# Kernel optimization log

Measured on AMD Instinct MI355X. Metric: run time of the kernel, lower is better.

## Reference

```python
import jax, jax.numpy as jnp
import numpy as np

B = 512          # batch of visual features
VF_D = 4096      # visual feature dim (VGG fc7)
HID_D = 2048     # hidden dim
EMB_D = 300      # order-embedding / label-vector dim
N_LABELS = 2000  # number of GT label vectors


def setup_inputs() -> dict:
    key = jax.random.key(0)
    ks = jax.random.split(key, 4)
    vfs = jax.random.normal(ks[0], (B, VF_D), dtype=jnp.float32)
    W1 = jax.random.normal(ks[1], (VF_D, HID_D), dtype=jnp.float32) * (1.0 / np.sqrt(VF_D))
    b1 = jnp.zeros((HID_D,), dtype=jnp.float32)
    W2 = jax.random.normal(ks[2], (HID_D, EMB_D), dtype=jnp.float32) * (1.0 / np.sqrt(HID_D))
    b2 = jnp.zeros((EMB_D,), dtype=jnp.float32)
    gt_label_vecs = jax.random.normal(ks[3], (N_LABELS, EMB_D), dtype=jnp.float32)
    return {"vfs": vfs, "W1": W1, "b1": b1, "W2": W2, "b2": b2,
            "gt_label_vecs": gt_label_vecs}


def reference(vfs, W1, b1, W2, b2, gt_label_vecs):
    # hidden_layer: ReLU -> (Dropout, identity at eval) -> Linear
    vf_hidden = jnp.dot(jax.nn.relu(vfs), W1) + b1            # [B, HID_D]
    # embedding_layer: ReLU -> Linear
    vf_emb = jnp.dot(jax.nn.relu(vf_hidden), W2) + b2         # [B, EMB_D]
    # order_sim(hypers=gt_label_vecs, hypos=vf_emb):
    #   score = -|| clamp(hypo - hyper, min=0) ||^2, batched over all pairs
    diff = jax.nn.relu(vf_emb[:, None, :] - gt_label_vecs[None, :, :])  # [B, N, D]
    score_stack = -jnp.sum(diff * diff, axis=-1)              # [B, N_LABELS]
    return score_stack, vf_emb
```

## Files before the change

### kernel.cpp

```cpp
#include <hip/hip_runtime.h>

#define B_SZ   512
#define VFD    4096
#define HIDD   2048
#define EMBD   300
#define NLAB   2000
#define NPAD   320

#define G1_SPLIT 4
#define G2_SPLIT 8

typedef __attribute__((ext_vector_type(8))) short short8x;
typedef __attribute__((ext_vector_type(4))) float f32x4;
typedef __attribute__((ext_vector_type(8))) unsigned short ushort8;
typedef __attribute__((ext_vector_type(4))) unsigned short ushort4x;

typedef const __attribute__((address_space(1))) unsigned int* gas_t;
typedef __attribute__((address_space(3))) unsigned int* las_t;

__device__ inline unsigned short f2bf(float x) {
    unsigned u = __float_as_uint(x);
    u += 0x7FFF + ((u >> 16) & 1);
    return (unsigned short)(u >> 16);
}

__global__ __launch_bounds__(256) void prep_kernel(
    const float* __restrict__ vfs, unsigned short* __restrict__ Xb,
    const float* __restrict__ W1, unsigned short* __restrict__ W1T,
    const float* __restrict__ W2, unsigned short* __restrict__ W2T)
{
    __shared__ float tile[64][65];
    const int tid = threadIdx.x;
    const int blk = blockIdx.x;

    if (blk < 1024) {
        const int i = (blk * 256 + tid) * 8;
        float4 a = *(const float4*)&vfs[i];
        float4 b = *(const float4*)&vfs[i + 4];
        ushort8 o;
        o[0] = f2bf(fmaxf(a.x, 0.f)); o[1] = f2bf(fmaxf(a.y, 0.f));
        o[2] = f2bf(fmaxf(a.z, 0.f)); o[3] = f2bf(fmaxf(a.w, 0.f));
        o[4] = f2bf(fmaxf(b.x, 0.f)); o[5] = f2bf(fmaxf(b.y, 0.f));
        o[6] = f2bf(fmaxf(b.z, 0.f)); o[7] = f2bf(fmaxf(b.w, 0.f));
        *(ushort8*)&Xb[i] = o;
        return;
    }

    const float* in; unsigned short* out; int N, ldK, bx, by;
    if (blk < 3072) {
        const int b = blk - 1024;
        in = W1; out = W1T; N = HIDD; ldK = VFD; bx = b & 31; by = b >> 5;
    } else {
        const int b = blk - 3072;
        in = W2; out = W2T; N = EMBD; ldK = HIDD; bx = b % 5; by = b / 5;
    }
    const int n0 = bx * 64, k0 = by * 64;

    #pragma unroll
    for (int i = 0; i < 4; ++i) {
        const int s = tid + 256 * i;
        const int kr = s >> 4, nc = (s & 15) * 4;
        float4 v = {0.f, 0.f, 0.f, 0.f};
        if (n0 + nc < N) v = *(const float4*)&in[(size_t)(k0 + kr) * N + n0 + nc];
        tile[kr][nc + 0] = v.x; tile[kr][nc + 1] = v.y;
        tile[kr][nc + 2] = v.z; tile[kr][nc + 3] = v.w;
    }
    __syncthreads();

    const int row = tid >> 2, kq = (tid & 3) * 16;
    ushort8 o0, o1;
    #pragma unroll
    for (int j = 0; j < 8; ++j) o0[j] = f2bf(tile[kq + j][row]);
    #pragma unroll
    for (int j = 0; j < 8; ++j) o1[j] = f2bf(tile[kq + 8 + j][row]);
    const size_t off = (size_t)(n0 + row) * ldK + k0 + kq;
    *(ushort8*)&out[off]     = o0;
    *(ushort8*)&out[off + 8] = o1;
}

template<int LDA, int LDB, int LDC, int KCHUNK>
__global__ __launch_bounds__(256) void gemm_bf16_kernel(
    const unsigned short* __restrict__ A,
    const unsigned short* __restrict__ Bt,
    float* __restrict__ Cpart, int M)
{
    __shared__ unsigned short As[2][2048];
    __shared__ unsigned short Bs[2][2048];

    const int tid = threadIdx.x;
    const int m0 = blockIdx.y * 64, n0 = blockIdx.x * 64;
    const int kbase = blockIdx.z * KCHUNK;

    const int soct = tid >> 6, srow = tid & 63;
    const unsigned short* ga = A  + (size_t)(m0 + srow) * LDA + kbase + soct * 8;
    const unsigned short* gb = Bt + (size_t)(n0 + srow) * LDB + kbase + soct * 8;

    const int lane = tid & 63;
    const int wave = tid >> 6;
    const int wm = (wave & 1) * 32;
    const int wn = (wave >> 1) * 32;
    const int q = lane >> 4, l15 = lane & 15;

    f32x4 acc00 = {0.f,0.f,0.f,0.f}, acc01 = {0.f,0.f,0.f,0.f};
    f32x4 acc10 = {0.f,0.f,0.f,0.f}, acc11 = {0.f,0.f,0.f,0.f};

    __builtin_amdgcn_global_load_lds((gas_t)(const void*)ga,
                                     (las_t)(void*)&As[0][tid * 8], 16, 0, 0);
    __builtin_amdgcn_global_load_lds((gas_t)(const void*)gb,
                                     (las_t)(void*)&Bs[0][tid * 8], 16, 0, 0);

    const int iters = KCHUNK / 32;
    for (int t = 0; t < iters; ++t) {
        const int cur = t & 1, nxt = cur ^ 1;
        __syncthreads();

        if (t + 1 < iters) {
            __builtin_amdgcn_global_load_lds((gas_t)(const void*)(ga + (t + 1) * 32),
                                             (las_t)(void*)&As[nxt][tid * 8], 16, 0, 0);
            __builtin_amdgcn_global_load_lds((gas_t)(const void*)(gb + (t + 1) * 32),
                                             (las_t)(void*)&Bs[nxt][tid * 8], 16, 0, 0);
        }

        short8x a0 = *(short8x*)&As[cur][(q * 64 + wm +      l15) * 8];
        short8x a1 = *(short8x*)&As[cur][(q * 64 + wm + 16 + l15) * 8];
        short8x b0 = *(short8x*)&Bs[cur][(q * 64 + wn +      l15) * 8];
        short8x b1 = *(short8x*)&Bs[cur][(q * 64 + wn + 16 + l15) * 8];
        acc00 = __builtin_amdgcn_mfma_f32_16x16x32_bf16(a0, b0, acc00, 0, 0, 0);
        acc01 = __builtin_amdgcn_mfma_f32_16x16x32_bf16(a0, b1, acc01, 0, 0, 0);
        acc10 = __builtin_amdgcn_mfma_f32_16x16x32_bf16(a1, b0, acc10, 0, 0, 0);
        acc11 = __builtin_amdgcn_mfma_f32_16x16x32_bf16(a1, b1, acc11, 0, 0, 0);
    }

    float* Cz = Cpart + (size_t)blockIdx.z * M * LDC;
    #pragma unroll
    for (int r = 0; r < 4; ++r) {
        const int rr = m0 + wm + q * 4 + r;
        const int cc = n0 + wn + l15;
        Cz[(size_t)rr * LDC + cc]             = acc00[r];
        Cz[(size_t)rr * LDC + cc + 16]        = acc01[r];
        Cz[(size_t)(rr + 16) * LDC + cc]      = acc10[r];
        Cz[(size_t)(rr + 16) * LDC + cc + 16] = acc11[r];
    }
}

__global__ __launch_bounds__(256) void reduce_h_kernel(
    const float* __restrict__ Hpart, const float* __restrict__ b1,
    unsigned short* __restrict__ Hb)
{
    const int i = (blockIdx.x * 256 + threadIdx.x) * 4;
    const int col = i & (HIDD - 1);
    float4 s = *(const float4*)&b1[col];
    #pragma unroll
    for (int z = 0; z < G1_SPLIT; ++z) {
        float4 p = *(const float4*)&Hpart[(size_t)z * B_SZ * HIDD + i];
        s.x += p.x; s.y += p.y; s.z += p.z; s.w += p.w;
    }
    ushort4x o;
    o[0] = f2bf(fmaxf(s.x, 0.f));
    o[1] = f2bf(fmaxf(s.y, 0.f));
    o[2] = f2bf(fmaxf(s.z, 0.f));
    o[3] = f2bf(fmaxf(s.w, 0.f));
    *(ushort4x*)&Hb[i] = o;
}

__global__ __launch_bounds__(256) void reduce_e_kernel(
    const float* __restrict__ Epart, const float* __restrict__ b2,
    float* __restrict__ E)
{
    const int gid = blockIdx.x * 256 + threadIdx.x;
    if (gid >= B_SZ * EMBD) return;
    const int m = gid / EMBD, n = gid - m * EMBD;
    float v = b2[n];
    #pragma unroll
    for (int z = 0; z < G2_SPLIT; ++z)
        v += Epart[(size_t)z * B_SZ * NPAD + m * NPAD + n];
    E[gid] = v;
}

__global__ __launch_bounds__(256) void scores_kernel(
    const float* __restrict__ E, const float* __restrict__ G,
    float* __restrict__ out)
{
    __shared__ float Es[32][68];
    __shared__ float Gs[64][68];

    const int tid = threadIdx.x;
    const int tx = tid & 15, ty = tid >> 4;
    const int n0 = blockIdx.x * 64, b0 = blockIdx.y * 32;

    float acc[2][4] = {};

    for (int dc = 0; dc < 320; dc += 64) {
        #pragma unroll
        for (int i = 0; i < 2; ++i) {
            const int s = tid + 256 * i;
            const int row = s >> 4, qd = (s & 15) * 4;
            const int d = dc + qd;
            float4 v = {0.f, 0.f, 0.f, 0.f};
            if (d < EMBD) v = *(const float4*)&E[(size_t)(b0 + row) * EMBD + d];
            *(float4*)&Es[row][qd] = v;
        }
        #pragma unroll
        for (int i = 0; i < 4; ++i) {
            const int s = tid + 256 * i;
            const int row = s >> 4, qd = (s & 15) * 4;
            const int d = dc + qd;
            const int n = n0 + row;
            float4 v = {0.f, 0.f, 0.f, 0.f};
            if (n < NLAB && d < EMBD) v = *(const float4*)&G[(size_t)n * EMBD + d];
            *(float4*)&Gs[row][qd] = v;
        }
        __syncthreads();

        #pragma unroll 4
        for (int d = 0; d < 64; d += 4) {
            float4 e0 = *(float4*)&Es[ty * 2][d];
            float4 e1 = *(float4*)&Es[ty * 2 + 1][d];
            #pragma unroll
            for (int r = 0; r < 4; ++r) {
                float4 g = *(float4*)&Gs[tx + 16 * r][d];
                float t0;
                t0 = fmaxf(e0.x - g.x, 0.f); acc[0][r] += t0 * t0;
                t0 = fmaxf(e0.y - g.y, 0.f); acc[0][r] += t0 * t0;
                t0 = fmaxf(e0.z - g.z, 0.f); acc[0][r] += t0 * t0;
                t0 = fmaxf(e0.w - g.w, 0.f); acc[0][r] += t0 * t0;
                t0 = fmaxf(e1.x - g.x, 0.f); acc[1][r] += t0 * t0;
                t0 = fmaxf(e1.y - g.y, 0.f); acc[1][r] += t0 * t0;
                t0 = fmaxf(e1.z - g.z, 0.f); acc[1][r] += t0 * t0;
                t0 = fmaxf(e1.w - g.w, 0.f); acc[1][r] += t0 * t0;
            }
        }
        __syncthreads();
    }

    #pragma unroll
    for (int p = 0; p < 2; ++p) {
        const int b = b0 + ty * 2 + p;
        #pragma unroll
        for (int r = 0; r < 4; ++r) {
            const int n = n0 + tx + 16 * r;
            if (n < NLAB) out[(size_t)b * NLAB + n] = -acc[p][r];
        }
    }
}

extern "C" void kernel_launch(void* const* d_in, const int* in_sizes, int n_in,
                              void* d_out, int out_size, void* d_ws, size_t ws_size,
                              hipStream_t stream)
{
    const float* vfs = (const float*)d_in[0];
    const float* W1  = (const float*)d_in[1];
    const float* b1  = (const float*)d_in[2];
    const float* W2  = (const float*)d_in[3];
    const float* b2  = (const float*)d_in[4];
    const float* G   = (const float*)d_in[5];

    float* out    = (float*)d_out;
    float* scores = out;
    float* E      = out + (size_t)B_SZ * NLAB;

    char* ws = (char*)d_ws;
    unsigned short* Xb  = (unsigned short*)(ws);
    unsigned short* W1T = (unsigned short*)(ws + 4194304);
    unsigned short* W2T = (unsigned short*)(ws + 20971520);
    unsigned short* Hb  = (unsigned short*)(ws + 22282240);
    float*          Hpart = (float*)(ws + 24379392);
    float*          Epart = (float*)(ws + 41156608);

    prep_kernel<<<3232, 256, 0, stream>>>(vfs, Xb, W1, W1T, W2, W2T);

    gemm_bf16_kernel<VFD, VFD, HIDD, VFD / G1_SPLIT>
        <<<dim3(32, 8, G1_SPLIT), 256, 0, stream>>>(Xb, W1T, Hpart, B_SZ);
    reduce_h_kernel<<<1024, 256, 0, stream>>>(Hpart, b1, Hb);

    gemm_bf16_kernel<HIDD, HIDD, NPAD, HIDD / G2_SPLIT>
        <<<dim3(5, 8, G2_SPLIT), 256, 0, stream>>>(Hb, W2T, Epart, B_SZ);
    reduce_e_kernel<<<600, 256, 0, stream>>>(Epart, b2, E);

    scores_kernel<<<dim3(32, 16), 256, 0, stream>>>(E, G, scores);
}
```

Measured before the change: 173.5 us.

## Split order-similarity score kernel over embedding dim with partial-sum combine

The score kernel is split across the embedding dimension into four slices, launching four times as many smaller blocks (128 threads, 4x4 outputs per thread) that write partial sums to workspace. A separate combine kernel adds the slices and negates them. E is now read straight from global memory instead of being staged in shared memory. The aim is more blocks and more work per thread for the previously low-occupancy grid of 512 blocks, at the cost of an extra launch and partial-sum traffic through workspace (reusing the Hpart region).

```diff
diff --git a/kernel.cpp b/kernel.cpp
--- a/kernel.cpp
+++ b/kernel.cpp
@@ -9,6 +9,7 @@
 
 #define G1_SPLIT 4
 #define G2_SPLIT 8
+#define SD_SPLIT 4
 
 typedef __attribute__((ext_vector_type(8))) short short8x;
 typedef __attribute__((ext_vector_type(4))) float f32x4;
@@ -177,34 +178,27 @@
     E[gid] = v;
 }
 
-__global__ __launch_bounds__(256) void scores_kernel(
+__global__ __launch_bounds__(128) void scores_part_kernel(
     const float* __restrict__ E, const float* __restrict__ G,
-    float* __restrict__ out)
-{
-    __shared__ float Es[32][68];
-    __shared__ float Gs[64][68];
+    float* __restrict__ part)
+{
+    __shared__ float Gs[64][44];
 
     const int tid = threadIdx.x;
     const int tx = tid & 15, ty = tid >> 4;
     const int n0 = blockIdx.x * 64, b0 = blockIdx.y * 32;
-
-    float acc[2][4] = {};
-
-    for (int dc = 0; dc < 320; dc += 64) {
+    const int dbase = blockIdx.z * (NPAD / SD_SPLIT);
+
+    float acc[4][4] = {};
+
+    for (int dc = 0; dc < NPAD / SD_SPLIT; dc += 40) {
+        const int d0 = dbase + dc;
+        __syncthreads();
         #pragma unroll
-        for (int i = 0; i < 2; ++i) {
-            const int s = tid + 256 * i;
-            const int row = s >> 4, qd = (s & 15) * 4;
-            const int d = dc + qd;
-            float4 v = {0.f, 0.f, 0.f, 0.f};
-            if (d < EMBD) v = *(const float4*)&E[(size_t)(b0 + row) * EMBD + d];
-            *(float4*)&Es[row][qd] = v;
-        }
-        #pragma unroll
-        for (int i = 0; i < 4; ++i) {
-            const int s = tid + 256 * i;
-            const int row = s >> 4, qd = (s & 15) * 4;
-            const int d = dc + qd;
+        for (int i = 0; i < 5; ++i) {
+            const int s = tid + 128 * i;
+            const int row = s / 10, qd = (s - row * 10) * 4;
+            const int d = d0 + qd;
             const int n = n0 + row;
             float4 v = {0.f, 0.f, 0.f, 0.f};
             if (n < NLAB && d < EMBD) v = *(const float4*)&G[(size_t)n * EMBD + d];
@@ -212,36 +206,57 @@
         }
         __syncthreads();
 
-        #pragma unroll 4
-        for (int d = 0; d < 64; d += 4) {
-            float4 e0 = *(float4*)&Es[ty * 2][d];
-            float4 e1 = *(float4*)&Es[ty * 2 + 1][d];
+        #pragma unroll 2
+        for (int d = 0; d < 40; d += 4) {
+            const int dd = d0 + d;
+            float4 e[4];
+            if (dd < EMBD) {
+                #pragma unroll
+                for (int r = 0; r < 4; ++r)
+                    e[r] = *(const float4*)&E[(size_t)(b0 + ty * 4 + r) * EMBD + dd];
+            } else {
+                #pragma unroll
+                for (int r = 0; r < 4; ++r) e[r] = make_float4(0.f, 0.f, 0.f, 0.f);
+            }
             #pragma unroll
-            for (int r = 0; r < 4; ++r) {
-                float4 g = *(float4*)&Gs[tx + 16 * r][d];
-                float t0;
-                t0 = fmaxf(e0.x - g.x, 0.f); acc[0][r] += t0 * t0;
-                t0 = fmaxf(e0.y - g.y, 0.f); acc[0][r] += t0 * t0;
-                t0 = fmaxf(e0.z - g.z, 0.f); acc[0][r] += t0 * t0;
-                t0 = fmaxf(e0.w - g.w, 0.f); acc[0][r] += t0 * t0;
-                t0 = fmaxf(e1.x - g.x, 0.f); acc[1][r] += t0 * t0;
-                t0 = fmaxf(e1.y - g.y, 0.f); acc[1][r] += t0 * t0;
-                t0 = fmaxf(e1.z - g.z, 0.f); acc[1][r] += t0 * t0;
-                t0 = fmaxf(e1.w - g.w, 0.f); acc[1][r] += t0 * t0;
+            for (int c = 0; c < 4; ++c) {
+                float4 g = *(float4*)&Gs[tx + 16 * c][d];
+                #pragma unroll
+                for (int r = 0; r < 4; ++r) {
+                    float t;
+                    t = fmaxf(e[r].x - g.x, 0.f); acc[r][c] += t * t;
+                    t = fmaxf(e[r].y - g.y, 0.f); acc[r][c] += t * t;
+                    t = fmaxf(e[r].z - g.z, 0.f); acc[r][c] += t * t;
+                    t = fmaxf(e[r].w - g.w, 0.f); acc[r][c] += t * t;
+                }
             }
         }
-        __syncthreads();
-    }
-
-    #pragma unroll
-    for (int p = 0; p < 2; ++p) {
-        const int b = b0 + ty * 2 + p;
+    }
+
+    float* pz = part + (size_t)blockIdx.z * B_SZ * NLAB;
+    #pragma unroll
+    for (int r = 0; r < 4; ++r) {
+        const int b = b0 + ty * 4 + r;
         #pragma unroll
-        for (int r = 0; r < 4; ++r) {
-            const int n = n0 + tx + 16 * r;
-            if (n < NLAB) out[(size_t)b * NLAB + n] = -acc[p][r];
-        }
-    }
+        for (int c = 0; c < 4; ++c) {
+            const int n = n0 + tx + 16 * c;
+            if (n < NLAB) pz[(size_t)b * NLAB + n] = acc[r][c];
+        }
+    }
+}
+
+__global__ __launch_bounds__(256) void scores_combine_kernel(
+    const float* __restrict__ part, float* __restrict__ scores)
+{
+    const int i = (blockIdx.x * 256 + threadIdx.x) * 4;
+    float4 s = {0.f, 0.f, 0.f, 0.f};
+    #pragma unroll
+    for (int z = 0; z < SD_SPLIT; ++z) {
+        float4 p = *(const float4*)&part[(size_t)z * B_SZ * NLAB + i];
+        s.x += p.x; s.y += p.y; s.z += p.z; s.w += p.w;
+    }
+    float4 o = make_float4(-s.x, -s.y, -s.z, -s.w);
+    *(float4*)&scores[i] = o;
 }
 
 extern "C" void kernel_launch(void* const* d_in, const int* in_sizes, int n_in,
@@ -266,6 +281,7 @@
     unsigned short* Hb  = (unsigned short*)(ws + 22282240);
     float*          Hpart = (float*)(ws + 24379392);
     float*          Epart = (float*)(ws + 41156608);
+    float*          Spart = (float*)(ws + 24379392);
 
     prep_kernel<<<3232, 256, 0, stream>>>(vfs, Xb, W1, W1T, W2, W2T);
 
@@ -277,5 +293,6 @@
         <<<dim3(5, 8, G2_SPLIT), 256, 0, stream>>>(Hb, W2T, Epart, B_SZ);
     reduce_e_kernel<<<600, 256, 0, stream>>>(Epart, b2, E);
 
-    scores_kernel<<<dim3(32, 16), 256, 0, stream>>>(E, G, scores);
-}
+    scores_part_kernel<<<dim3(32, 16, SD_SPLIT), 128, 0, stream>>>(E, G, Spart);
+    scores_combine_kernel<<<1000, 256, 0, stream>>>(Spart, scores);
+}
```

Measured after the change: 178.2 us. 2.7% more time.
